# Optimization experiments

Hardware: AMD Instinct MI355X
Metric: run time of the kernel (lower is better)

Reference implementation:

```python
import jax, jax.numpy as jnp
import numpy as np

D_MODEL = 1024
N_HEADS = 16
D_HEAD = D_MODEL // N_HEADS


def setup_inputs() -> dict:
    key = jax.random.key(0)
    ks = jax.random.split(key, 9)
    s = 1.0 / np.sqrt(D_MODEL)
    def lin(kw, kb):
        W = jax.random.uniform(kw, (D_MODEL, D_MODEL), jnp.float32, -s, s)
        b = jax.random.uniform(kb, (D_MODEL,), jnp.float32, -s, s)
        return W, b
    Wq, bq = lin(ks[0], ks[1])
    Wk, bk = lin(ks[2], ks[3])
    Wv, bv = lin(ks[4], ks[5])
    Wo, bo = lin(ks[6], ks[7])
    x = jax.random.normal(ks[8], (4, 2048, D_MODEL), jnp.float32)
    return {"x": x, "Wq": Wq, "bq": bq, "Wk": Wk, "bk": bk,
            "Wv": Wv, "bv": bv, "Wo": Wo, "bo": bo}


def reference(x, Wq, bq, Wk, bk, Wv, bv, Wo, bo):
    B, T, C = x.shape
    # torch Linear: y = x @ W.T + b
    Q = x @ Wq.T + bq
    K = x @ Wk.T + bk
    V = x @ Wv.T + bv
    # [B, H, T, Dh]
    Q = Q.reshape(B, T, N_HEADS, D_HEAD).transpose(0, 2, 1, 3)
    K = K.reshape(B, T, N_HEADS, D_HEAD).transpose(0, 2, 1, 3)
    V = V.reshape(B, T, N_HEADS, D_HEAD).transpose(0, 2, 1, 3)
    scale = jnp.float32(np.sqrt(D_HEAD))
    scores = jnp.einsum('bhqd,bhkd->bhqk', Q, K) / scale
    causal = jnp.tril(jnp.ones((T, T), dtype=bool))  # True where allowed
    scores = jnp.where(causal, scores, jnp.float32(-jnp.inf))
    attn = jax.nn.softmax(scores, axis=-1)
    out = jnp.einsum('bhqk,bhkd->bhqd', attn, V)
    out = out.transpose(0, 2, 1, 3).reshape(B, T, C)
    return out @ Wo.T + bo
```

## Files before the change

### kernel.cpp

```cpp
#include <hip/hip_runtime.h>
#include <hip/hip_bf16.h>


typedef float f32x4 __attribute__((ext_vector_type(4)));
typedef __bf16 bf16x8 __attribute__((ext_vector_type(8)));

#define DEVI __device__ __forceinline__

#define QSCALE 0.1803368801111204f

template<int N> struct IC { static constexpr int value = N; };

DEVI ushort f2b(float x) {
  __hip_bfloat16 h = __float2bfloat16(x);
  return __builtin_bit_cast(ushort, h);
}

DEVI unsigned int pkbf(float a, float b) {
#if __has_builtin(__builtin_amdgcn_cvt_pk_bf16_f32)
  typedef __bf16 bf16x2 __attribute__((ext_vector_type(2)));
  bf16x2 r = __builtin_amdgcn_cvt_pk_bf16_f32(a, b);
  return __builtin_bit_cast(unsigned int, r);
#else
  return (unsigned int)f2b(a) | ((unsigned int)f2b(b) << 16);
#endif
}

DEVI bf16x8 ldsFrag(const ushort* p) {
  return __builtin_bit_cast(bf16x8, *(const uint4*)p);
}

DEVI f32x4 mfma16(bf16x8 a, bf16x8 b, f32x4 c) {
  return __builtin_amdgcn_mfma_f32_16x16x32_bf16(a, b, c, 0, 0, 0);
}

DEVI void gload_lds16(const ushort* g, ushort* l) {
  __builtin_amdgcn_global_load_lds(
      (const __attribute__((address_space(1))) unsigned int*)g,
      (__attribute__((address_space(3))) unsigned int*)l, 16, 0, 0);
}

__global__ void k_cvtAll(const float4* __restrict__ x,
                         const float4* __restrict__ w0, const float4* __restrict__ w1,
                         const float4* __restrict__ w2, const float4* __restrict__ w3,
                         ushort4* __restrict__ xb, ushort4* __restrict__ wcat) {
  const int blk = blockIdx.x;
  const int i = blk * 256 + threadIdx.x;
  float4 f;
  ushort4* dst;
  int di;
  if (blk < 8192) {
    f = x[i]; dst = xb; di = i;
  } else {
    const int wi = i - 8192 * 256;
    const int sel = wi >> 18;
    const float4* src = (sel == 0) ? w0 : (sel == 1) ? w1 : (sel == 2) ? w2 : w3;
    f = src[wi & 262143]; dst = wcat; di = wi;
  }
  ushort4 o;
  o.x = f2b(f.x); o.y = f2b(f.y); o.z = f2b(f.z); o.w = f2b(f.w);
  dst[di] = o;
}

template<int MODE>
__global__ __launch_bounds__(256)
void k_gemm(const ushort* __restrict__ A, const ushort* __restrict__ W,
            const float* __restrict__ b0, const float* __restrict__ b1,
            const float* __restrict__ b2, float* __restrict__ outF,
            ushort* __restrict__ oQ, ushort* __restrict__ oK, ushort* __restrict__ oV) {
  __shared__ ushort As[128 * 64];
  __shared__ ushort Bs[128 * 64];
  const int tid = threadIdx.x;
  const int wave = tid >> 6, lane = tid & 63;
  const int col = lane & 15, quad = lane >> 4;
  const int id = blockIdx.x;
  const int s_ = id >> 3;
  const int m0 = ((id & 7) * 8 + (s_ & 7)) * 128;
  const int n0 = (s_ >> 3) * 128;
  const int wm = (wave >> 1) * 64, wn = (wave & 1) * 64;
  f32x4 acc[4][4] = {};

  const int grow = lane >> 3;
  const int gchunk = ((lane & 7) ^ grow) * 8;
  const ushort* Ag = A + (size_t)(m0 + wave * 8 + grow) * 1024 + gchunk;
  const ushort* Wg = W + (size_t)(n0 + wave * 8 + grow) * 1024 + gchunk;
  ushort* AsW = &As[wave * 512];
  ushort* BsW = &Bs[wave * 512];

  const int matId = (MODE == 0) ? (n0 >> 10) : 0;
  const int cswz = col & 7;

  auto kloop = [&](auto swc) {
    constexpr bool SW = (decltype(swc)::value != 0);
    for (int k0 = 0; k0 < 1024; k0 += 64) {
      __syncthreads();
#pragma unroll
      for (int g = 0; g < 4; ++g) {
        gload_lds16(Ag + (size_t)g * 32 * 1024 + k0, AsW + g * 2048);
        gload_lds16(Wg + (size_t)g * 32 * 1024 + k0, BsW + g * 2048);
      }
      __syncthreads();
#pragma unroll
      for (int kk = 0; kk < 2; ++kk) {
        bf16x8 af[4], bfr[4];
#pragma unroll
        for (int i = 0; i < 4; ++i)
          af[i] = ldsFrag(&As[(wm + i * 16 + col) * 64 + (((kk * 4 + quad) ^ cswz) * 8)]);
#pragma unroll
        for (int j = 0; j < 4; ++j)
          bfr[j] = ldsFrag(&Bs[(wn + j * 16 + col) * 64 + (((kk * 4 + quad) ^ cswz) * 8)]);
#pragma unroll
        for (int i = 0; i < 4; ++i)
#pragma unroll
          for (int j = 0; j < 4; ++j) {
            if constexpr (SW)
              acc[i][j] = mfma16(bfr[j], af[i], acc[i][j]);
            else
              acc[i][j] = mfma16(af[i], bfr[j], acc[i][j]);
          }
      }
    }
  };

  if (MODE == 1 || matId < 2) kloop(IC<1>{}); else kloop(IC<0>{});

  if (MODE == 1) {
#pragma unroll
    for (int j = 0; j < 4; ++j) {
      const int nb = n0 + wn + j * 16 + quad * 4;
      const float4 bb = *(const float4*)&b0[nb];
#pragma unroll
      for (int i = 0; i < 4; ++i) {
        const int m = m0 + wm + i * 16 + col;
        float4 v;
        v.x = acc[i][j][0] + bb.x;
        v.y = acc[i][j][1] + bb.y;
        v.z = acc[i][j][2] + bb.z;
        v.w = acc[i][j][3] + bb.w;
        *(float4*)&outF[(size_t)m * 1024 + nb] = v;
      }
    }
  } else if (matId < 2) {
    ushort* dst = (matId == 0) ? oQ : oK;
    const float* bias = (matId == 0) ? b0 : b1;
    const float sc = (matId == 0) ? QSCALE : 1.0f;
#pragma unroll
    for (int j = 0; j < 4; ++j) {
      const int nl = ((n0 & 1023) + wn + j * 16 + quad * 4);
      const int h = nl >> 6, dh0 = nl & 63;
      const float4 bb = *(const float4*)&bias[nl];
#pragma unroll
      for (int i = 0; i < 4; ++i) {
        const int m = m0 + wm + i * 16 + col;
        const int b = m >> 11, t = m & 2047;
        ushort4 pk;
        pk.x = f2b((acc[i][j][0] + bb.x) * sc);
        pk.y = f2b((acc[i][j][1] + bb.y) * sc);
        pk.z = f2b((acc[i][j][2] + bb.z) * sc);
        pk.w = f2b((acc[i][j][3] + bb.w) * sc);
        *(ushort4*)&dst[(((size_t)(b * 16 + h) * 2048) + t) * 64 + dh0] = pk;
      }
    }
  } else {
#pragma unroll
    for (int j = 0; j < 4; ++j) {
      const int nl = ((n0 & 1023) + wn + j * 16 + col);
      const int h = nl >> 6, dh = nl & 63;
      const float bn = b2[nl];
#pragma unroll
      for (int i = 0; i < 4; ++i) {
        const int mBase = m0 + wm + i * 16 + quad * 4;
        const int b = mBase >> 11, t = mBase & 2047;
        ushort4 pk;
        pk.x = f2b(acc[i][j][0] + bn);
        pk.y = f2b(acc[i][j][1] + bn);
        pk.z = f2b(acc[i][j][2] + bn);
        pk.w = f2b(acc[i][j][3] + bn);
        *(ushort4*)&oV[(((size_t)(b * 16 + h) * 64) + dh) * 2048 + t] = pk;
      }
    }
  }
}

__global__ __launch_bounds__(512, 1)
void k_attn(const ushort* __restrict__ Q, const ushort* __restrict__ K,
            const ushort* __restrict__ Vt, ushort* __restrict__ AO) {
  __shared__ ushort Ks[2 * 4096];
  __shared__ ushort Vs[2 * 4096];
  __shared__ ushort Os[512];
  __shared__ ushort Ps[16 * 16 * 72];
  const int tid = threadIdx.x;
  const int wave = tid >> 6, lane = tid & 63;
  const int col = lane & 15, quad = lane >> 4;
  const int id = blockIdx.x;
  const int bh = (id & 7) * 8 + ((id >> 3) & 7);
  const int pr = id >> 6;
  const ushort* Qg = Q + (size_t)bh * 2048 * 64;
  const ushort* Kg = K + (size_t)bh * 2048 * 64;
  const ushort* Vg = Vt + (size_t)bh * 64 * 2048;

  if (tid < 128) {
    const ushort one = 0x3F80;
    ushort4 zv;
    if (tid < 8) { zv.x = one; zv.y = one; zv.z = one; zv.w = one; }
    else         { zv.x = 0;   zv.y = 0;   zv.z = 0;   zv.w = 0;   }
    *(ushort4*)&Os[tid * 4] = zv;
  }

  const int grow = lane >> 3;
  const int gchunk = ((lane & 7) ^ grow) * 8;
  const int cswz = col & 7;
  ushort* Pw0 = &Ps[((wave * 2 + 0) * 16 + col) * 72];
  ushort* Pw1 = &Ps[((wave * 2 + 1) * 16 + col) * 72];

  for (int pp = 0; pp < 2; ++pp) {
    const int t = pp ? (7 - pr) : pr;
    const int q0 = t * 256;

    bf16x8 qf[2][2];
#pragma unroll
    for (int s = 0; s < 2; ++s) {
      const ushort* p = Qg + (q0 + wave * 32 + s * 16 + col) * 64 + quad * 8;
      qf[s][0] = __builtin_bit_cast(bf16x8, *(const uint4*)p);
      qf[s][1] = __builtin_bit_cast(bf16x8, *(const uint4*)(p + 32));
    }

    f32x4 o[2][4] = {};
    f32x4 la[2] = {};

    const ushort* kPtr = Kg + (wave * 8 + grow) * 64 + gchunk;
    const ushort* vPtr = Vg + (size_t)(wave * 8 + grow) * 2048 + gchunk;

    auto stage = [&](auto bufc) {
      constexpr int BUF = decltype(bufc)::value;
      gload_lds16(kPtr, &Ks[BUF * 4096 + wave * 512]);
      gload_lds16(vPtr, &Vs[BUF * 4096 + wave * 512]);
      kPtr += 64 * 64;
      vPtr += 64;
    };

    auto step = [&](auto bufc, auto maskc, int j0) {
      constexpr int BUF = decltype(bufc)::value;
      constexpr bool MASKED = (decltype(maskc)::value != 0);
      const ushort* Kb = &Ks[BUF * 4096];
      const ushort* Vb = &Vs[BUF * 4096];
      bf16x8 kf[4][2];
#pragma unroll
      for (int i = 0; i < 4; ++i) {
        kf[i][0] = ldsFrag(&Kb[(i * 16 + col) * 64 + (((0 * 4 + quad) ^ cswz) * 8)]);
        kf[i][1] = ldsFrag(&Kb[(i * 16 + col) * 64 + (((1 * 4 + quad) ^ cswz) * 8)]);
      }
#pragma unroll
      for (int s = 0; s < 2; ++s) {
        ushort* Pw = s ? Pw1 : Pw0;
        const int dlim = MASKED ? (q0 + wave * 32 + s * 16 + col - j0 - quad * 4) : 0;
#pragma unroll
        for (int i = 0; i < 4; ++i) {
          f32x4 z = {0.f, 0.f, 0.f, 0.f};
          f32x4 sv = mfma16(kf[i][0], qf[s][0], z);
          sv = mfma16(kf[i][1], qf[s][1], sv);
          if (MASKED) {
#pragma unroll
            for (int r = 0; r < 4; ++r)
              if (i * 16 + r > dlim) sv[r] = -1e30f;
          }
          f32x4 pv;
#pragma unroll
          for (int r = 0; r < 4; ++r) pv[r] = __builtin_amdgcn_exp2f(sv[r]);
          uint2 pk;
          pk.x = pkbf(pv[0], pv[1]);
          pk.y = pkbf(pv[2], pv[3]);
          *(uint2*)&Pw[i * 16 + quad * 4] = pk;
        }
      }
      bf16x8 osf = ldsFrag(&Os[col * 32 + quad * 8]);
#pragma unroll
      for (int c = 0; c < 2; ++c) {
        bf16x8 pb0 = ldsFrag(&Pw0[c * 32 + quad * 8]);
        bf16x8 pb1 = ldsFrag(&Pw1[c * 32 + quad * 8]);
        la[0] = mfma16(osf, pb0, la[0]);
        la[1] = mfma16(osf, pb1, la[1]);
#pragma unroll
        for (int i = 0; i < 4; ++i) {
          bf16x8 vf = ldsFrag(&Vb[(i * 16 + col) * 64 + (((c * 4 + quad) ^ cswz) * 8)]);
          o[0][i] = mfma16(vf, pb0, o[0][i]);
          o[1][i] = mfma16(vf, pb1, o[1][i]);
        }
      }
    };

    __syncthreads();
    stage(IC<0>{});
    for (int it2 = 0; it2 < 2 * t; ++it2) {
      __syncthreads();
      stage(IC<1>{});
      step(IC<0>{}, IC<0>{}, 0);
      __syncthreads();
      stage(IC<0>{});
      step(IC<1>{}, IC<0>{}, 0);
    }
    __syncthreads();
    stage(IC<1>{});
    step(IC<0>{}, IC<1>{}, q0);
    __syncthreads();
    stage(IC<0>{});
    if (wave >= 2) step(IC<1>{}, IC<1>{}, q0 + 64);
    __syncthreads();
    stage(IC<1>{});
    if (wave >= 4) step(IC<0>{}, IC<1>{}, q0 + 128);
    __syncthreads();
    if (wave >= 6) step(IC<1>{}, IC<1>{}, q0 + 192);

    const float invs[2] = {1.0f / __shfl(la[0][0], col), 1.0f / __shfl(la[1][0], col)};
    const int b = bh >> 4, h = bh & 15;
#pragma unroll
    for (int s = 0; s < 2; ++s) {
      const float inv = invs[s];
      const int tq = q0 + wave * 32 + s * 16 + col;
      ushort* dst = AO + (size_t)(b * 2048 + tq) * 1024 + h * 64;
#pragma unroll
      for (int i = 0; i < 4; ++i) {
        f32x4 v = o[s][i];
        ushort4 pk;
        pk.x = f2b(v[0] * inv);
        pk.y = f2b(v[1] * inv);
        pk.z = f2b(v[2] * inv);
        pk.w = f2b(v[3] * inv);
        *(ushort4*)&dst[i * 16 + quad * 4] = pk;
      }
    }
  }
}

extern "C" void kernel_launch(void* const* d_in, const int* in_sizes, int n_in,
                              void* d_out, int out_size, void* d_ws, size_t ws_size,
                              hipStream_t stream) {
  const float* x  = (const float*)d_in[0];
  const float* Wq = (const float*)d_in[1];
  const float* bq = (const float*)d_in[2];
  const float* Wk = (const float*)d_in[3];
  const float* bk = (const float*)d_in[4];
  const float* Wv = (const float*)d_in[5];
  const float* bv = (const float*)d_in[6];
  const float* Wo = (const float*)d_in[7];
  const float* bo = (const float*)d_in[8];
  float* out = (float*)d_out;

  char* ws = (char*)d_ws;
  ushort* xb    = (ushort*)ws;
  ushort* Wcat  = (ushort*)(ws + (size_t)16 * 1024 * 1024);
  ushort* Wob   = Wcat + (size_t)3 * 1024 * 1024;
  ushort* Qh    = (ushort*)(ws + (size_t)24 * 1024 * 1024);
  ushort* Kh    = Qh + (size_t)8192 * 1024;
  ushort* Vt    = Kh + (size_t)8192 * 1024;
  ushort* AO    = Vt + (size_t)8192 * 1024;

  k_cvtAll<<<12288, 256, 0, stream>>>((const float4*)x,
                                      (const float4*)Wq, (const float4*)Wk,
                                      (const float4*)Wv, (const float4*)Wo,
                                      (ushort4*)xb, (ushort4*)Wcat);

  k_gemm<0><<<1536, 256, 0, stream>>>(xb, Wcat, bq, bk, bv, nullptr, Qh, Kh, Vt);

  k_attn<<<256, 512, 0, stream>>>(Qh, Kh, Vt, AO);

  k_gemm<1><<<512, 256, 0, stream>>>(AO, Wob, bo, nullptr, nullptr, out,
                                     nullptr, nullptr, nullptr);
}
```

Baseline: 247.6 us.

## Triple-buffer GEMM K-loop with 128x256 tiles and 512-thread blocks

Reworks the projection GEMM kernel to use 512-thread blocks over 128x256 output tiles. K-tiles are triple-buffered in LDS, so global-to-LDS loads for step k+2 are issued while MFMAs run on step k. Explicit sched barriers, vmcnt waits and setprio give finer control over how loads and MFMAs interleave. The aim is to hide global load latency and cut the per-iteration double __syncthreads stalls. In exchange, LDS use per block grows a lot (about 144KB), which may limit occupancy. The hand-written waitcnt counts also have to match the number of loads in flight exactly.

```diff
diff --git a/kernel.cpp b/kernel.cpp
--- a/kernel.cpp
+++ b/kernel.cpp
@@ -39,6 +39,10 @@
       (const __attribute__((address_space(1))) unsigned int*)g,
       (__attribute__((address_space(3))) unsigned int*)l, 16, 0, 0);
 }
+
+#define SBAR() do { __builtin_amdgcn_sched_barrier(0); \
+                    __builtin_amdgcn_s_barrier();      \
+                    __builtin_amdgcn_sched_barrier(0); } while (0)
 
 __global__ void k_cvtAll(const float4* __restrict__ x,
                          const float4* __restrict__ w0, const float4* __restrict__ w1,
@@ -63,63 +67,94 @@
 }
 
 template<int MODE>
-__global__ __launch_bounds__(256)
+__global__ __launch_bounds__(512, 2)
 void k_gemm(const ushort* __restrict__ A, const ushort* __restrict__ W,
             const float* __restrict__ b0, const float* __restrict__ b1,
             const float* __restrict__ b2, float* __restrict__ outF,
             ushort* __restrict__ oQ, ushort* __restrict__ oK, ushort* __restrict__ oV) {
-  __shared__ ushort As[128 * 64];
-  __shared__ ushort Bs[128 * 64];
+  __shared__ ushort As[3 * 128 * 64];
+  __shared__ ushort Bs[3 * 256 * 64];
   const int tid = threadIdx.x;
   const int wave = tid >> 6, lane = tid & 63;
   const int col = lane & 15, quad = lane >> 4;
   const int id = blockIdx.x;
   const int s_ = id >> 3;
   const int m0 = ((id & 7) * 8 + (s_ & 7)) * 128;
-  const int n0 = (s_ >> 3) * 128;
-  const int wm = (wave >> 1) * 64, wn = (wave & 1) * 64;
+  const int n0 = (s_ >> 3) * 256;
+  const int wm = (wave >> 2) * 64, wn = (wave & 3) * 64;
   f32x4 acc[4][4] = {};
 
   const int grow = lane >> 3;
   const int gchunk = ((lane & 7) ^ grow) * 8;
-  const ushort* Ag = A + (size_t)(m0 + wave * 8 + grow) * 1024 + gchunk;
-  const ushort* Wg = W + (size_t)(n0 + wave * 8 + grow) * 1024 + gchunk;
-  ushort* AsW = &As[wave * 512];
-  ushort* BsW = &Bs[wave * 512];
+  const int cswz = col & 7;
+  const ushort* Ag = A + (size_t)(m0 + wave * 16 + grow) * 1024 + gchunk;
+  const ushort* Wg = W + (size_t)(n0 + wave * 32 + grow) * 1024 + gchunk;
+  ushort* AsW = &As[wave * 1024];
+  ushort* BsW = &Bs[wave * 2048];
 
   const int matId = (MODE == 0) ? (n0 >> 10) : 0;
-  const int cswz = col & 7;
+
+  auto stageA = [&](int ks, int sb) {
+    gload_lds16(Ag + ks,        AsW + sb * 8192);
+    gload_lds16(Ag + ks + 8192, AsW + sb * 8192 + 512);
+  };
+  auto stageBh = [&](int ks, int sb, int h) {
+    const ushort* sp = Wg + ks + h * 16384;
+    ushort* dp = BsW + sb * 16384 + h * 1024;
+    gload_lds16(sp,        dp);
+    gload_lds16(sp + 8192, dp + 512);
+  };
 
   auto kloop = [&](auto swc) {
-    constexpr bool SW = (decltype(swc)::value != 0);
-    for (int k0 = 0; k0 < 1024; k0 += 64) {
-      __syncthreads();
-#pragma unroll
-      for (int g = 0; g < 4; ++g) {
-        gload_lds16(Ag + (size_t)g * 32 * 1024 + k0, AsW + g * 2048);
-        gload_lds16(Wg + (size_t)g * 32 * 1024 + k0, BsW + g * 2048);
-      }
-      __syncthreads();
-#pragma unroll
-      for (int kk = 0; kk < 2; ++kk) {
-        bf16x8 af[4], bfr[4];
-#pragma unroll
-        for (int i = 0; i < 4; ++i)
-          af[i] = ldsFrag(&As[(wm + i * 16 + col) * 64 + (((kk * 4 + quad) ^ cswz) * 8)]);
-#pragma unroll
-        for (int j = 0; j < 4; ++j)
-          bfr[j] = ldsFrag(&Bs[(wn + j * 16 + col) * 64 + (((kk * 4 + quad) ^ cswz) * 8)]);
-#pragma unroll
-        for (int i = 0; i < 4; ++i)
-#pragma unroll
-          for (int j = 0; j < 4; ++j) {
-            if constexpr (SW)
-              acc[i][j] = mfma16(bfr[j], af[i], acc[i][j]);
-            else
-              acc[i][j] = mfma16(af[i], bfr[j], acc[i][j]);
-          }
-      }
-    }
+    auto phase = [&](int cur, int kk, auto stagef) {
+      const int ko = ((kk * 4 + quad) ^ cswz) * 8;
+      const ushort* Ab = &As[cur * 8192];
+      const ushort* Bb = &Bs[cur * 16384];
+      bf16x8 af[4], bfr[4];
+#pragma unroll
+      for (int i = 0; i < 4; ++i)
+        af[i] = ldsFrag(&Ab[(wm + i * 16 + col) * 64 + ko]);
+#pragma unroll
+      for (int j = 0; j < 4; ++j)
+        bfr[j] = ldsFrag(&Bb[(wn + j * 16 + col) * 64 + ko]);
+      stagef();
+      SBAR();
+      __builtin_amdgcn_s_setprio(1);
+#pragma unroll
+      for (int i = 0; i < 4; ++i)
+#pragma unroll
+        for (int j = 0; j < 4; ++j) {
+          if constexpr (decltype(swc)::value != 0)
+            acc[i][j] = mfma16(bfr[j], af[i], acc[i][j]);
+          else
+            acc[i][j] = mfma16(af[i], bfr[j], acc[i][j]);
+        }
+      __builtin_amdgcn_s_setprio(0);
+    };
+
+    stageA(0, 0);  stageBh(0, 0, 0);  stageBh(0, 0, 1);
+    stageA(64, 1); stageBh(64, 1, 0); stageBh(64, 1, 1);
+    asm volatile("s_waitcnt vmcnt(6)" ::: "memory");
+    SBAR();
+
+    int r0 = 0, r1 = 1, r2 = 2;
+    for (int t = 0; t < 14; ++t) {
+      const int ks = (t + 2) * 64;
+      phase(r0, 0, [&] { stageA(ks, r2); stageBh(ks, r2, 0); });
+      SBAR();
+      phase(r0, 1, [&] { stageBh(ks, r2, 1); });
+      asm volatile("s_waitcnt vmcnt(6)" ::: "memory");
+      SBAR();
+      const int tmp = r0; r0 = r1; r1 = r2; r2 = tmp;
+    }
+    phase(r0, 0, [&] {});
+    SBAR();
+    phase(r0, 1, [&] {});
+    asm volatile("s_waitcnt vmcnt(0)" ::: "memory");
+    SBAR();
+    phase(r1, 0, [&] {});
+    SBAR();
+    phase(r1, 1, [&] {});
   };
 
   if (MODE == 1 || matId < 2) kloop(IC<1>{}); else kloop(IC<0>{});
@@ -360,10 +395,10 @@
                                       (const float4*)Wv, (const float4*)Wo,
                                       (ushort4*)xb, (ushort4*)Wcat);
 
-  k_gemm<0><<<1536, 256, 0, stream>>>(xb, Wcat, bq, bk, bv, nullptr, Qh, Kh, Vt);
+  k_gemm<0><<<768, 512, 0, stream>>>(xb, Wcat, bq, bk, bv, nullptr, Qh, Kh, Vt);
 
   k_attn<<<256, 512, 0, stream>>>(Qh, Kh, Vt, AO);
 
-  k_gemm<1><<<512, 256, 0, stream>>>(AO, Wob, bo, nullptr, nullptr, out,
+  k_gemm<1><<<256, 512, 0, stream>>>(AO, Wob, bo, nullptr, nullptr, out,
                                      nullptr, nullptr, nullptr);
 }
```

Result: no change. 245.2 us (-1.0%).

## Restructure GEMM with larger tiles, double-buffered LDS pipeline, split V projection

Applied to the files above, without the earlier changes.

Rewrites the GEMM kernel to use 512-thread blocks with wider N tiles (512 for Q/K, 256 for V and output) and a double-buffered shared-memory pipeline. The next tile's loads are issued before the current tile's MFMAs, with a single barrier per k-step and scheduling/priority hints. The V projection moves into its own launch (MODE 2) so each kernel instantiation has a fixed operand order, which removes the runtime branch. The aim is more data reuse per tile and less load latency exposed at barriers, at the cost of more registers, a larger LDS footprint and an extra kernel launch.

```diff
diff --git a/kernel.cpp b/kernel.cpp
--- a/kernel.cpp
+++ b/kernel.cpp
@@ -63,70 +63,94 @@
 }
 
 template<int MODE>
-__global__ __launch_bounds__(256)
+__global__ __launch_bounds__(512, 2)
 void k_gemm(const ushort* __restrict__ A, const ushort* __restrict__ W,
             const float* __restrict__ b0, const float* __restrict__ b1,
-            const float* __restrict__ b2, float* __restrict__ outF,
+            float* __restrict__ outF,
             ushort* __restrict__ oQ, ushort* __restrict__ oK, ushort* __restrict__ oV) {
-  __shared__ ushort As[128 * 64];
-  __shared__ ushort Bs[128 * 64];
+  constexpr int BN = (MODE == 0) ? 512 : 256;
+  constexpr int NJ = BN / 64;
+  constexpr int ROWS = 128 + BN;
+  constexpr int U = ROWS / 64;
+  constexpr bool SWAP = (MODE != 2);
+  __shared__ ushort S[2][ROWS * 64];
   const int tid = threadIdx.x;
   const int wave = tid >> 6, lane = tid & 63;
   const int col = lane & 15, quad = lane >> 4;
   const int id = blockIdx.x;
-  const int s_ = id >> 3;
-  const int m0 = ((id & 7) * 8 + (s_ & 7)) * 128;
-  const int n0 = (s_ >> 3) * 128;
-  const int wm = (wave >> 1) * 64, wn = (wave & 1) * 64;
-  f32x4 acc[4][4] = {};
-
+  const int L = (id & 7) * 32 + (id >> 3);
+  const int m0 = (L & 63) * 128;
+  const int n0 = (L >> 6) * BN;
+  const int wm = (wave >> 2) * 64;
+  const int wn = (wave & 3) * (BN / 4);
   const int grow = lane >> 3;
   const int gchunk = ((lane & 7) ^ grow) * 8;
-  const ushort* Ag = A + (size_t)(m0 + wave * 8 + grow) * 1024 + gchunk;
-  const ushort* Wg = W + (size_t)(n0 + wave * 8 + grow) * 1024 + gchunk;
-  ushort* AsW = &As[wave * 512];
-  ushort* BsW = &Bs[wave * 512];
-
-  const int matId = (MODE == 0) ? (n0 >> 10) : 0;
   const int cswz = col & 7;
 
-  auto kloop = [&](auto swc) {
-    constexpr bool SW = (decltype(swc)::value != 0);
-    for (int k0 = 0; k0 < 1024; k0 += 64) {
-      __syncthreads();
-#pragma unroll
-      for (int g = 0; g < 4; ++g) {
-        gload_lds16(Ag + (size_t)g * 32 * 1024 + k0, AsW + g * 2048);
-        gload_lds16(Wg + (size_t)g * 32 * 1024 + k0, BsW + g * 2048);
-      }
-      __syncthreads();
-#pragma unroll
-      for (int kk = 0; kk < 2; ++kk) {
-        bf16x8 af[4], bfr[4];
-#pragma unroll
-        for (int i = 0; i < 4; ++i)
-          af[i] = ldsFrag(&As[(wm + i * 16 + col) * 64 + (((kk * 4 + quad) ^ cswz) * 8)]);
-#pragma unroll
-        for (int j = 0; j < 4; ++j)
-          bfr[j] = ldsFrag(&Bs[(wn + j * 16 + col) * 64 + (((kk * 4 + quad) ^ cswz) * 8)]);
-#pragma unroll
-        for (int i = 0; i < 4; ++i)
-#pragma unroll
-          for (int j = 0; j < 4; ++j) {
-            if constexpr (SW)
-              acc[i][j] = mfma16(bfr[j], af[i], acc[i][j]);
-            else
-              acc[i][j] = mfma16(af[i], bfr[j], acc[i][j]);
-          }
-      }
-    }
+  const int wdiff = (int)(W - A);
+  int goff[U];
+#pragma unroll
+  for (int g = 0; g < U; ++g) {
+    const int r = wave * (U * 8) + g * 8 + grow;
+    goff[g] = (r < 128) ? ((m0 + r) * 1024 + gchunk)
+                        : (wdiff + (n0 + r - 128) * 1024 + gchunk);
+  }
+
+  f32x4 acc[4][NJ] = {};
+
+  auto stage = [&](int t1) {
+    const int ks = t1 * 64;
+    ushort* d = &S[t1 & 1][wave * (U * 512)];
+#pragma unroll
+    for (int g = 0; g < U; ++g)
+      gload_lds16(A + goff[g] + ks, d + g * 512);
   };
 
-  if (MODE == 1 || matId < 2) kloop(IC<1>{}); else kloop(IC<0>{});
-
-  if (MODE == 1) {
-#pragma unroll
-    for (int j = 0; j < 4; ++j) {
+  auto phase = [&](int buf, int kk, auto stg) {
+    const int ko = ((kk * 4 + quad) ^ cswz) * 8;
+    const ushort* Sb = S[buf];
+    stg();
+    bf16x8 af[4], bfr[NJ];
+#pragma unroll
+    for (int i = 0; i < 4; ++i)
+      af[i] = ldsFrag(&Sb[(wm + i * 16 + col) * 64 + ko]);
+#pragma unroll
+    for (int j = 0; j < NJ; ++j)
+      bfr[j] = ldsFrag(&Sb[(128 + wn + j * 16 + col) * 64 + ko]);
+    __builtin_amdgcn_sched_barrier(0);
+    __builtin_amdgcn_s_setprio(1);
+#pragma unroll
+    for (int i = 0; i < 4; ++i)
+#pragma unroll
+      for (int j = 0; j < NJ; ++j) {
+        if constexpr (SWAP)
+          acc[i][j] = mfma16(bfr[j], af[i], acc[i][j]);
+        else
+          acc[i][j] = mfma16(af[i], bfr[j], acc[i][j]);
+      }
+    __builtin_amdgcn_s_setprio(0);
+    __builtin_amdgcn_sched_barrier(0);
+  };
+
+  stage(0);
+  asm volatile("s_waitcnt vmcnt(0)" ::: "memory");
+  __builtin_amdgcn_s_barrier();
+
+  for (int t = 0; t < 15; ++t) {
+    const int buf = t & 1;
+    phase(buf, 0, [&] { stage(t + 1); });
+    phase(buf, 1, [&] {});
+    asm volatile("s_waitcnt vmcnt(0)" ::: "memory");
+    __builtin_amdgcn_sched_barrier(0);
+    __builtin_amdgcn_s_barrier();
+    __builtin_amdgcn_sched_barrier(0);
+  }
+  phase(1, 0, [&] {});
+  phase(1, 1, [&] {});
+
+  if constexpr (MODE == 1) {
+#pragma unroll
+    for (int j = 0; j < NJ; ++j) {
       const int nb = n0 + wn + j * 16 + quad * 4;
       const float4 bb = *(const float4*)&b0[nb];
 #pragma unroll
@@ -140,43 +164,44 @@
         *(float4*)&outF[(size_t)m * 1024 + nb] = v;
       }
     }
-  } else if (matId < 2) {
+  } else if constexpr (MODE == 0) {
+    const int matId = n0 >> 10;
     ushort* dst = (matId == 0) ? oQ : oK;
     const float* bias = (matId == 0) ? b0 : b1;
     const float sc = (matId == 0) ? QSCALE : 1.0f;
 #pragma unroll
-    for (int j = 0; j < 4; ++j) {
-      const int nl = ((n0 & 1023) + wn + j * 16 + quad * 4);
+    for (int j = 0; j < NJ; ++j) {
+      const int nl = (n0 & 1023) + wn + j * 16 + quad * 4;
       const int h = nl >> 6, dh0 = nl & 63;
       const float4 bb = *(const float4*)&bias[nl];
 #pragma unroll
       for (int i = 0; i < 4; ++i) {
         const int m = m0 + wm + i * 16 + col;
-        const int b = m >> 11, t = m & 2047;
+        const int b = m >> 11, tt = m & 2047;
         ushort4 pk;
         pk.x = f2b((acc[i][j][0] + bb.x) * sc);
         pk.y = f2b((acc[i][j][1] + bb.y) * sc);
         pk.z = f2b((acc[i][j][2] + bb.z) * sc);
         pk.w = f2b((acc[i][j][3] + bb.w) * sc);
-        *(ushort4*)&dst[(((size_t)(b * 16 + h) * 2048) + t) * 64 + dh0] = pk;
+        *(ushort4*)&dst[(((size_t)(b * 16 + h) * 2048) + tt) * 64 + dh0] = pk;
       }
     }
   } else {
 #pragma unroll
-    for (int j = 0; j < 4; ++j) {
-      const int nl = ((n0 & 1023) + wn + j * 16 + col);
+    for (int j = 0; j < NJ; ++j) {
+      const int nl = n0 + wn + j * 16 + col;
       const int h = nl >> 6, dh = nl & 63;
-      const float bn = b2[nl];
+      const float bn = b0[nl];
 #pragma unroll
       for (int i = 0; i < 4; ++i) {
         const int mBase = m0 + wm + i * 16 + quad * 4;
-        const int b = mBase >> 11, t = mBase & 2047;
+        const int b = mBase >> 11, tt = mBase & 2047;
         ushort4 pk;
         pk.x = f2b(acc[i][j][0] + bn);
         pk.y = f2b(acc[i][j][1] + bn);
         pk.z = f2b(acc[i][j][2] + bn);
         pk.w = f2b(acc[i][j][3] + bn);
-        *(ushort4*)&oV[(((size_t)(b * 16 + h) * 64) + dh) * 2048 + t] = pk;
+        *(ushort4*)&oV[(((size_t)(b * 16 + h) * 64) + dh) * 2048 + tt] = pk;
       }
     }
   }
@@ -349,6 +374,7 @@
   char* ws = (char*)d_ws;
   ushort* xb    = (ushort*)ws;
   ushort* Wcat  = (ushort*)(ws + (size_t)16 * 1024 * 1024);
+  ushort* Wvb   = Wcat + (size_t)2 * 1024 * 1024;
   ushort* Wob   = Wcat + (size_t)3 * 1024 * 1024;
   ushort* Qh    = (ushort*)(ws + (size_t)24 * 1024 * 1024);
   ushort* Kh    = Qh + (size_t)8192 * 1024;
@@ -360,10 +386,13 @@
                                       (const float4*)Wv, (const float4*)Wo,
                                       (ushort4*)xb, (ushort4*)Wcat);
 
-  k_gemm<0><<<1536, 256, 0, stream>>>(xb, Wcat, bq, bk, bv, nullptr, Qh, Kh, Vt);
+  k_gemm<0><<<256, 512, 0, stream>>>(xb, Wcat, bq, bk, nullptr, Qh, Kh, nullptr);
+
+  k_gemm<2><<<256, 512, 0, stream>>>(xb, Wvb, bv, nullptr, nullptr,
+                                     nullptr, nullptr, Vt);
 
   k_attn<<<256, 512, 0, stream>>>(Qh, Kh, Vt, AO);
 
-  k_gemm<1><<<512, 256, 0, stream>>>(AO, Wob, bo, nullptr, nullptr, out,
+  k_gemm<1><<<256, 512, 0, stream>>>(AO, Wob, bo, nullptr, out,
                                      nullptr, nullptr, nullptr);
 }
```

Result: slower. 253.2 us (+2.3%).
